# Performance work log

Measured on AMD Instinct MI355X. Metric: run time of the kernel, lower is better.

The kernel has to match this reference:

```python
import jax, jax.numpy as jnp
import numpy as np

# Static graph layout: B equal-size graphs so per-graph k is static under jit.
B = 64          # number of graphs
N_PER = 1024    # nodes per graph
RATIO = 0.5
K = max(1, int(RATIO * N_PER))  # 512 nodes kept per graph
MULTIPLIER = 1.0
N = B * N_PER   # 65536 total nodes
E = 2_097_152   # total edges
F_IN = 256
F_E = 16


def setup_inputs() -> dict:
    key = jax.random.key(0)
    k1, k2, k3, k4 = jax.random.split(key, 4)
    x = jax.random.normal(k1, (N, F_IN), dtype=jnp.float32)
    edge_index = jax.random.randint(k2, (2, E), 0, N, dtype=jnp.int32)
    edge_attr = jax.random.normal(k3, (E, F_E), dtype=jnp.float32)
    batch = jnp.repeat(jnp.arange(B, dtype=jnp.int32), N_PER)  # sorted, equal sizes
    # Linear(in_channels, 1) params (PyTorch default init style)
    W = jax.random.uniform(k4, (1, F_IN), dtype=jnp.float32,
                           minval=-1.0, maxval=1.0) / jnp.sqrt(F_IN)
    b = jnp.zeros((1,), dtype=jnp.float32)
    return {"x": x, "edge_index": edge_index, "edge_attr": edge_attr,
            "batch": batch, "W": W, "b": b}


def reference(x, edge_index, edge_attr, batch, W, b):
    # score = multiplier * tanh(proj(x))  -> [N]
    score = MULTIPLIER * jnp.tanh(x @ W.T + b)[:, 0]

    # Per-graph top-k (graphs are contiguous, equal size -> reshape + top_k)
    _, idx = jax.lax.top_k(score.reshape(B, N_PER), K)        # [B, K], desc order
    offsets = (jnp.arange(B, dtype=idx.dtype) * N_PER)[:, None]
    perm = (idx + offsets).reshape(-1)                          # [B*K] global node ids
    batch_out = jnp.repeat(jnp.arange(B, dtype=batch.dtype), K)

    # Gate kept node features by their score
    x_out = x[perm] * score[perm][:, None]                      # [B*K, F_IN]

    # filter_adj: keep edges whose both endpoints survive, remap node ids
    mask = jnp.zeros((N,), dtype=bool).at[perm].set(True)
    row, col = edge_index[0], edge_index[1]
    edge_mask = mask[row] & mask[col]                           # [E]
    node_map = jnp.zeros((N,), dtype=jnp.int32).at[perm].set(
        jnp.arange(B * K, dtype=jnp.int32))
    # jit-friendly: fixed-size outputs; invalid edges marked -1 / zeroed
    ei_new = jnp.where(edge_mask[None, :], node_map[edge_index], -1)
    ea_new = jnp.where(edge_mask[:, None], edge_attr, 0.0)

    return (x_out, ei_new, ea_new, batch_out, perm, score, edge_mask)
```

## Files before the change

### kernel.cpp

```cpp
#include <hip/hip_runtime.h>
#include <math.h>

#define BGRAPH 64
#define N_PER  1024
#define KSEL   512
#define NTOT   65536
#define EDG    2097152
#define FIN    256
#define FE     16

#define OFF_XOUT   0
#define OFF_EI     8388608
#define OFF_EA     12582912
#define OFF_BATCH  46137344
#define OFF_PERM   46170112
#define OFF_SCORE  46202880
#define OFF_EMASK  46268416

#define WS_DOTS_OFF 65536

__global__ __launch_bounds__(256) void score_kernel(
    const float* __restrict__ x, const float* __restrict__ W,
    const float* __restrict__ bptr, float* __restrict__ score_out,
    double* __restrict__ dot_out) {
  int wave = threadIdx.x >> 6;
  int lane = threadIdx.x & 63;
  int node = blockIdx.x * 4 + wave;
  const float4* xr = reinterpret_cast<const float4*>(x + (size_t)node * FIN);
  const float4* wr = reinterpret_cast<const float4*>(W);
  float4 xv = xr[lane];
  float4 wv = wr[lane];
  double p = (double)xv.x * (double)wv.x + (double)xv.y * (double)wv.y +
             (double)xv.z * (double)wv.z + (double)xv.w * (double)wv.w;
#pragma unroll
  for (int off = 32; off >= 1; off >>= 1) p += __shfl_xor(p, off, 64);
  if (lane == 0) {
    double z = p + (double)bptr[0];
    dot_out[node]   = z;
    score_out[node] = tanhf((float)z);
  }
}

__global__ __launch_bounds__(1024) void topk_kernel(
    const double* __restrict__ dots, float* __restrict__ perm_out,
    float* __restrict__ batch_out, int* __restrict__ node_map) {
  __shared__ double sk[N_PER];
  __shared__ int    si[N_PER];
  int b = blockIdx.x;
  int t = threadIdx.x;
  int base = b * N_PER;
  double key = dots[base + t];
  int    idx = t;
  node_map[base + t] = -1;
  for (int k = 2; k <= N_PER; k <<= 1) {
    for (int j = k >> 1; j > 0; j >>= 1) {
      bool lower = (t & j) == 0;
      bool dirUp = (t & k) == 0;
      double okey; int oidx;
      if (j >= 64) {
        sk[t] = key; si[t] = idx;
        __syncthreads();
        okey = sk[t ^ j]; oidx = si[t ^ j];
        __syncthreads();
      } else {
        okey = __shfl_xor(key, j, 64);
        oidx = __shfl_xor(idx, j, 64);
      }
      bool own_prec = (key > okey) || (key == okey && idx < oidx);
      bool want_prec = (lower == dirUp);
      if (own_prec != want_prec) { key = okey; idx = oidx; }
    }
  }
  if (t < KSEL) {
    int g   = base + idx;
    int gid = b * KSEL + t;
    perm_out[gid]  = (float)g;
    batch_out[gid] = (float)b;
    node_map[g]    = gid;
  }
}

__global__ __launch_bounds__(256) void gather_kernel(
    const float* __restrict__ x, const float* __restrict__ perm_f,
    const float* __restrict__ score, float* __restrict__ xout) {
  int wave = threadIdx.x >> 6;
  int lane = threadIdx.x & 63;
  int r = blockIdx.x * 4 + wave;
  int g = (int)perm_f[r];
  float s = score[g];
  float4 v = reinterpret_cast<const float4*>(x + (size_t)g * FIN)[lane];
  float4 o;
  o.x = v.x * s; o.y = v.y * s; o.z = v.z * s; o.w = v.w * s;
  reinterpret_cast<float4*>(xout + (size_t)r * FIN)[lane] = o;
}

__global__ __launch_bounds__(256) void edge_kernel(
    const int* __restrict__ ei, const int* __restrict__ node_map,
    const float* __restrict__ ea, float* __restrict__ ei_out,
    float* __restrict__ emask_out, float* __restrict__ ea_out) {
  __shared__ float smask[256];
  int t = threadIdx.x;
  int e0 = blockIdx.x * 256;
  int e = e0 + t;
  int r = ei[e];
  int c = ei[EDG + e];
  int nr = node_map[r];
  int nc = node_map[c];
  bool m = (nr >= 0) && (nc >= 0);
  ei_out[e]       = m ? (float)nr : -1.0f;
  ei_out[EDG + e] = m ? (float)nc : -1.0f;
  float mf = m ? 1.0f : 0.0f;
  emask_out[e] = mf;
  smask[t]     = mf;
  __syncthreads();
  const float4* ea4 = reinterpret_cast<const float4*>(ea) + (size_t)e0 * 4;
  float4*      out4 = reinterpret_cast<float4*>(ea_out)   + (size_t)e0 * 4;
#pragma unroll
  for (int q = 0; q < 4; ++q) {
    int fi = q * 256 + t;
    float mm = smask[fi >> 2];
    float4 v = make_float4(0.f, 0.f, 0.f, 0.f);
    if (mm != 0.0f) v = ea4[fi];
    out4[fi] = v;
  }
}

extern "C" void kernel_launch(void* const* d_in, const int* in_sizes, int n_in,
                              void* d_out, int out_size, void* d_ws, size_t ws_size,
                              hipStream_t stream) {
  const float* x  = (const float*)d_in[0];
  const int*   ei = (const int*)d_in[1];
  const float* ea = (const float*)d_in[2];
  const float* W  = (const float*)d_in[4];
  const float* bb = (const float*)d_in[5];

  float* out       = (float*)d_out;
  float* xout      = out + OFF_XOUT;
  float* ei_out    = out + OFF_EI;
  float* ea_out    = out + OFF_EA;
  float* batch_out = out + OFF_BATCH;
  float* perm_out  = out + OFF_PERM;
  float* score_out = out + OFF_SCORE;
  float* emask_out = out + OFF_EMASK;

  int*    node_map = (int*)d_ws;
  double* dots     = (double*)((int*)d_ws + WS_DOTS_OFF);

  score_kernel <<<NTOT / 4, 256, 0, stream>>>(x, W, bb, score_out, dots);
  topk_kernel  <<<BGRAPH, 1024, 0, stream>>>(dots, perm_out, batch_out, node_map);
  gather_kernel<<<(BGRAPH * KSEL) / 4, 256, 0, stream>>>(x, perm_out, score_out, xout);
  edge_kernel  <<<EDG / 256, 256, 0, stream>>>(ei, node_map, ea, ei_out, emask_out, ea_out);
}
```

Before: 112.4 us.

## Split edge kernel into vectorized index pass and batched attr-mask pass

Replaces the single edge kernel with two kernels. The first handles four edges per thread using int4 loads of the edge indices and float4 stores of remapped ids and the mask. The second reads the mask back from the output buffer and zeros or copies edge attributes, issuing eight float4 loads per thread to raise memory-level parallelism. The split removes the shared-memory barrier but adds a launch and a re-read of the mask array.

```diff
diff --git a/kernel.cpp b/kernel.cpp
--- a/kernel.cpp
+++ b/kernel.cpp
@@ -94,34 +94,55 @@
   reinterpret_cast<float4*>(xout + (size_t)r * FIN)[lane] = o;
 }
 
-__global__ __launch_bounds__(256) void edge_kernel(
+__global__ __launch_bounds__(256) void edgeA_kernel(
     const int* __restrict__ ei, const int* __restrict__ node_map,
-    const float* __restrict__ ea, float* __restrict__ ei_out,
-    float* __restrict__ emask_out, float* __restrict__ ea_out) {
-  __shared__ float smask[256];
+    float* __restrict__ ei_out, float* __restrict__ emask_out) {
+  int t = blockIdx.x * 256 + threadIdx.x;
+  int4 r4 = reinterpret_cast<const int4*>(ei)[t];
+  int4 c4 = reinterpret_cast<const int4*>(ei + EDG)[t];
+  int nr0 = node_map[r4.x], nr1 = node_map[r4.y];
+  int nr2 = node_map[r4.z], nr3 = node_map[r4.w];
+  int nc0 = node_map[c4.x], nc1 = node_map[c4.y];
+  int nc2 = node_map[c4.z], nc3 = node_map[c4.w];
+  bool m0 = (nr0 >= 0) && (nc0 >= 0);
+  bool m1 = (nr1 >= 0) && (nc1 >= 0);
+  bool m2 = (nr2 >= 0) && (nc2 >= 0);
+  bool m3 = (nr3 >= 0) && (nc3 >= 0);
+  float4 ro = make_float4(m0 ? (float)nr0 : -1.0f, m1 ? (float)nr1 : -1.0f,
+                          m2 ? (float)nr2 : -1.0f, m3 ? (float)nr3 : -1.0f);
+  float4 co = make_float4(m0 ? (float)nc0 : -1.0f, m1 ? (float)nc1 : -1.0f,
+                          m2 ? (float)nc2 : -1.0f, m3 ? (float)nc3 : -1.0f);
+  float4 mo = make_float4(m0 ? 1.0f : 0.0f, m1 ? 1.0f : 0.0f,
+                          m2 ? 1.0f : 0.0f, m3 ? 1.0f : 0.0f);
+  reinterpret_cast<float4*>(ei_out)[t]       = ro;
+  reinterpret_cast<float4*>(ei_out + EDG)[t] = co;
+  reinterpret_cast<float4*>(emask_out)[t]    = mo;
+}
+
+__global__ __launch_bounds__(256) void edgeB_kernel(
+    const float* __restrict__ ea, const float* __restrict__ emask,
+    float* __restrict__ ea_out) {
   int t = threadIdx.x;
-  int e0 = blockIdx.x * 256;
-  int e = e0 + t;
-  int r = ei[e];
-  int c = ei[EDG + e];
-  int nr = node_map[r];
-  int nc = node_map[c];
-  bool m = (nr >= 0) && (nc >= 0);
-  ei_out[e]       = m ? (float)nr : -1.0f;
-  ei_out[EDG + e] = m ? (float)nc : -1.0f;
-  float mf = m ? 1.0f : 0.0f;
-  emask_out[e] = mf;
-  smask[t]     = mf;
-  __syncthreads();
-  const float4* ea4 = reinterpret_cast<const float4*>(ea) + (size_t)e0 * 4;
-  float4*      out4 = reinterpret_cast<float4*>(ea_out)   + (size_t)e0 * 4;
+  int f0 = blockIdx.x * 2048;
+  const float4* ea4 = reinterpret_cast<const float4*>(ea);
+  float4*      out4 = reinterpret_cast<float4*>(ea_out);
+  float mm[8];
 #pragma unroll
-  for (int q = 0; q < 4; ++q) {
-    int fi = q * 256 + t;
-    float mm = smask[fi >> 2];
-    float4 v = make_float4(0.f, 0.f, 0.f, 0.f);
-    if (mm != 0.0f) v = ea4[fi];
-    out4[fi] = v;
+  for (int q = 0; q < 8; ++q) {
+    int fi = f0 + q * 256 + t;
+    mm[q] = emask[fi >> 2];
+  }
+  float4 v[8];
+#pragma unroll
+  for (int q = 0; q < 8; ++q) {
+    int fi = f0 + q * 256 + t;
+    v[q] = make_float4(0.f, 0.f, 0.f, 0.f);
+    if (mm[q] != 0.0f) v[q] = ea4[fi];
+  }
+#pragma unroll
+  for (int q = 0; q < 8; ++q) {
+    int fi = f0 + q * 256 + t;
+    out4[fi] = v[q];
   }
 }
 
@@ -149,5 +170,6 @@
   score_kernel <<<NTOT / 4, 256, 0, stream>>>(x, W, bb, score_out, dots);
   topk_kernel  <<<BGRAPH, 1024, 0, stream>>>(dots, perm_out, batch_out, node_map);
   gather_kernel<<<(BGRAPH * KSEL) / 4, 256, 0, stream>>>(x, perm_out, score_out, xout);
-  edge_kernel  <<<EDG / 256, 256, 0, stream>>>(ei, node_map, ea, ei_out, emask_out, ea_out);
+  edgeA_kernel <<<EDG / 4 / 256, 256, 0, stream>>>(ei, node_map, ei_out, emask_out);
+  edgeB_kernel <<<(EDG * 4) / 2048, 256, 0, stream>>>(ea, emask_out, ea_out);
 }
```

New measurement: 106.4 us. -5.4%, faster.
